# Optimization experiments

Hardware: AMD Instinct MI355X
Metric: run time of the kernel (lower is better)

The kernel has to match this reference:

```python
import jax, jax.numpy as jnp
import numpy as np

B, T, C = 4, 2048, 1024
N_HEAD = 16
HEAD = C // N_HEAD  # 64


def setup_inputs() -> dict:
    key = jax.random.key(0)
    k1, k2, k3 = jax.random.split(key, 3)
    x = jax.random.normal(k1, (B, T, C), dtype=jnp.float32)
    w_attn = jax.random.normal(k2, (C, 3 * C), dtype=jnp.float32) * (1.0 / np.sqrt(C))
    w_proj = jax.random.normal(k3, (C, C), dtype=jnp.float32) * (1.0 / np.sqrt(C))
    return {"x": x, "w_attn": w_attn, "w_proj": w_proj}


def reference(x, w_attn, w_proj):
    b, t, c = x.shape
    qkv = x @ w_attn  # [B,T,3C]
    q, k, v = jnp.split(qkv, 3, axis=-1)
    # [B,T,H,D] -> [B,H,T,D]
    q = q.reshape(b, t, N_HEAD, HEAD).transpose(0, 2, 1, 3)
    k = k.reshape(b, t, N_HEAD, HEAD).transpose(0, 2, 1, 3)
    v = v.reshape(b, t, N_HEAD, HEAD).transpose(0, 2, 1, 3)
    scale = 1.0 / np.sqrt(HEAD).astype(np.float32)
    attn = jnp.einsum('bhqd,bhkd->bhqk', q, k) * scale  # [B,H,T,T]
    causal = jnp.tril(jnp.ones((t, t), dtype=bool))
    attn = jnp.where(causal[None, None], attn, -jnp.inf)
    sm = jax.nn.softmax(attn, axis=-1)
    out = jnp.einsum('bhqk,bhkd->bhqd', sm, v)  # [B,H,T,D]
    out = out.transpose(0, 2, 1, 3).reshape(b, t, c)
    return out @ w_proj
```

## Files before the change

### kernel.cpp

```cpp
#include <hip/hip_runtime.h>
#include <stdint.h>

typedef unsigned short u16;
typedef __bf16 bf16x8 __attribute__((ext_vector_type(8)));
typedef float f32x4 __attribute__((ext_vector_type(4)));
typedef float f32x16 __attribute__((ext_vector_type(16)));

#define B_ 4
#define T_ 2048
#define C_ 1024
#define NH_ 16
#define HD_ 64
#define M_ (B_ * T_)
#define N1_ (3 * C_)
#define NQK_ 2048

__device__ inline u16 f2bf(float f) {
    uint32_t u = __float_as_uint(f);
    u += 0x7FFFu + ((u >> 16) & 1u);
    return (u16)(u >> 16);
}

__device__ inline bf16x8 ld_bf16x8(const u16* p) {
    return *(const bf16x8*)(const void*)p;
}

__device__ inline uint32_t cvtpk_bf16(float a, float b) {
    uint32_t r;
    asm("v_cvt_pk_bf16_f32 %0, %1, %2" : "=v"(r) : "v"(a), "v"(b));
    return r;
}

__device__ inline float exp2_fast(float x) {
    float r;
    asm("v_exp_f32 %0, %1" : "=v"(r) : "v"(x));
    return r;
}

__device__ inline void gload16(const u16* g, u16* l) {
    __builtin_amdgcn_global_load_lds(
        (const __attribute__((address_space(1))) uint32_t*)g,
        (__attribute__((address_space(3))) uint32_t*)l, 16, 0, 0);
}

__global__ void f32_to_bf16_k(const float* __restrict__ in, u16* __restrict__ out, int n) {
    int i = (blockIdx.x * blockDim.x + threadIdx.x) * 4;
    int stride = gridDim.x * blockDim.x * 4;
    for (; i < n; i += stride) {
        float4 v = *(const float4*)(in + i);
        uint2 o;
        o.x = (uint32_t)f2bf(v.x) | ((uint32_t)f2bf(v.y) << 16);
        o.y = (uint32_t)f2bf(v.z) | ((uint32_t)f2bf(v.w) << 16);
        *(uint2*)(out + i) = o;
    }
}

__global__ void transpose_f32_bf16_k(const float* __restrict__ in, u16* __restrict__ out,
                                     int R, int Cc, int scaleRows, float scale) {
    __shared__ float tile[32][33];
    int c0 = blockIdx.x * 32, r0 = blockIdx.y * 32;
    int tx = threadIdx.x, ty = threadIdx.y;
#pragma unroll
    for (int i = 0; i < 4; ++i)
        tile[ty + i * 8][tx] = in[(size_t)(r0 + ty + i * 8) * Cc + c0 + tx];
    __syncthreads();
#pragma unroll
    for (int i = 0; i < 4; ++i) {
        int orow = c0 + ty + i * 8;
        float v = tile[tx][ty + i * 8];
        if (orow < scaleRows) v *= scale;
        out[(size_t)orow * R + r0 + tx] = f2bf(v);
    }
}

template <int MODE>
__global__ __launch_bounds__(256) void gemm_bt_k(const u16* __restrict__ A,
                                                 const u16* __restrict__ Bt,
                                                 void* __restrict__ Cp,
                                                 u16* __restrict__ Vp,
                                                 int M, int N, int K) {
    __shared__ u16 As[128 * 32];
    __shared__ u16 Bs[128 * 32];
    const int t = threadIdx.x;
    const int w = t >> 6, l = t & 63;
    const int wr = w >> 1, wc = w & 1;
    const int lr = l & 15, lg = l >> 4;
    const int R0 = blockIdx.x * 128, C0 = blockIdx.y * 128;

    const int sr = t >> 2;
    const int sc = (t & 3) * 8;
    const u16* Ag  = A  + (size_t)(R0 + sr) * K + sc;
    const u16* Ag2 = Ag + (size_t)64 * K;
    const u16* Bg  = Bt + (size_t)(C0 + sr) * K + sc;
    const u16* Bg2 = Bg + (size_t)64 * K;

    f32x4 acc[4][4] = {};
    const int nk = K / 32;

    for (int kt = 0; kt < nk; ++kt) {
        __syncthreads();
        gload16(Ag  + (size_t)kt * 32, As + t * 8);
        gload16(Ag2 + (size_t)kt * 32, As + t * 8 + 2048);
        gload16(Bg  + (size_t)kt * 32, Bs + t * 8);
        gload16(Bg2 + (size_t)kt * 32, Bs + t * 8 + 2048);
        __syncthreads();

        bf16x8 af[4], bfr[4];
#pragma unroll
        for (int mi = 0; mi < 4; ++mi)
            af[mi] = ld_bf16x8(As + (wr * 64 + mi * 16 + lr) * 32 + lg * 8);
#pragma unroll
        for (int nj = 0; nj < 4; ++nj)
            bfr[nj] = ld_bf16x8(Bs + (wc * 64 + nj * 16 + lr) * 32 + lg * 8);
#pragma unroll
        for (int mi = 0; mi < 4; ++mi)
#pragma unroll
            for (int nj = 0; nj < 4; ++nj)
                acc[mi][nj] = __builtin_amdgcn_mfma_f32_16x16x32_bf16(af[mi], bfr[nj],
                                                                      acc[mi][nj], 0, 0, 0);
    }

    if (MODE == 2 && C0 >= 2048) {
#pragma unroll
        for (int mi = 0; mi < 4; ++mi) {
            int row = R0 + wr * 64 + mi * 16 + lg * 4;
            int bb = row >> 11, tt = row & 2047;
#pragma unroll
            for (int nj = 0; nj < 4; ++nj) {
                int cv = C0 - 2048 + wc * 64 + nj * 16 + lr;
                int hh = cv >> 6, dd = cv & 63;
                ushort4 pk;
                pk.x = f2bf(acc[mi][nj][0]);
                pk.y = f2bf(acc[mi][nj][1]);
                pk.z = f2bf(acc[mi][nj][2]);
                pk.w = f2bf(acc[mi][nj][3]);
                *(ushort4*)(Vp + (((size_t)bb * NH_ + hh) * HD_ + dd) * (size_t)T_ + tt) = pk;
            }
        }
    } else {
#pragma unroll
        for (int mi = 0; mi < 4; ++mi) {
            int row = R0 + wr * 64 + mi * 16 + lg * 4;
#pragma unroll
            for (int nj = 0; nj < 4; ++nj) {
                int col = C0 + wc * 64 + nj * 16 + lr;
#pragma unroll
                for (int r = 0; r < 4; ++r) {
                    if (MODE == 0)
                        ((float*)Cp)[(size_t)(row + r) * N + col] = acc[mi][nj][r];
                    else
                        ((u16*)Cp)[(size_t)(row + r) * NQK_ + col] = f2bf(acc[mi][nj][r]);
                }
            }
        }
    }
}

__global__ __launch_bounds__(256, 2) void attn_fwd_k(const u16* __restrict__ qk,
                                                     const u16* __restrict__ vT,
                                                     u16* __restrict__ attO) {
    __shared__ u16 Ks[2][64 * 64];
    __shared__ u16 Vs[2][64 * 64];

    const int t = threadIdx.x;
    const int w = t >> 6, l = t & 63;
    const int r0 = l & 31, hi = l >> 5;
    const int lin = blockIdx.x;
    const int bh = (lin & 7) * 8 + ((lin >> 3) & 7);
    const int pj = lin >> 6;
    const int b = bh >> 4, h = bh & 15;
    const u16* qkB = qk + (size_t)b * T_ * NQK_;

    const int sr = t >> 3;
    const int sof = ((t & 7) * 8) ^ ((sr & 7) << 3);
    const u16* gK = qkB + (size_t)sr * NQK_ + C_ + h * HD_ + sof;
    const u16* gV = vT + ((size_t)bh * HD_ + sr) * (size_t)T_ + sof;

    for (int jj = 0; jj < 2; ++jj) {
        const int J = jj ? pj : (15 - pj);
        const int qW = J * 128 + w * 32;
        const int nt = 2 * J + 2;

        bf16x8 qf[4];
        {
            const u16* qp = qkB + (size_t)(qW + r0) * NQK_ + h * HD_ + hi * 8;
#pragma unroll
            for (int dc = 0; dc < 4; ++dc) qf[dc] = ld_bf16x8(qp + dc * 16);
        }

        f32x16 acc0 = {}, acc1 = {};
        float m = -1e30f, lsum = 0.f;

        gload16(gK, Ks[0] + t * 8);
        gload16(gK + (size_t)32 * NQK_, Ks[0] + t * 8 + 2048);
        gload16(gV, Vs[0] + t * 8);
        gload16(gV + (size_t)32 * T_, Vs[0] + t * 8 + 2048);
        __syncthreads();

        for (int kt = 0; kt < nt; ++kt) {
            const int kv = kt * 64;
            if (kt + 1 < nt) {
                u16* dK = Ks[(kt + 1) & 1];
                u16* dV = Vs[(kt + 1) & 1];
                gload16(gK + (size_t)(kv + 64) * NQK_, dK + t * 8);
                gload16(gK + (size_t)(kv + 96) * NQK_, dK + t * 8 + 2048);
                gload16(gV + (kv + 64), dV + t * 8);
                gload16(gV + (size_t)32 * T_ + (kv + 64), dV + t * 8 + 2048);
            }
            const u16* Kb = Ks[kt & 1];
            const u16* Vb = Vs[kt & 1];

            if (kv <= qW) {
                const bool diag = (kv + 64 > qW);
                const bool up = (!diag) || (w & 1);

                f32x16 s0 = {}, s1 = {};
                __builtin_amdgcn_s_setprio(1);
#pragma unroll
                for (int dc = 0; dc < 4; ++dc) {
                    int off = (dc * 32 + hi * 16) ^ ((r0 & 7) << 4);
                    bf16x8 k0 = ld_bf16x8((const u16*)((const char*)Kb + r0 * 128 + off));
                    s0 = __builtin_amdgcn_mfma_f32_32x32x16_bf16(k0, qf[dc], s0, 0, 0, 0);
                    if (up) {
                        bf16x8 k1 = ld_bf16x8((const u16*)((const char*)Kb + r0 * 128 + 4096 + off));
                        s1 = __builtin_amdgcn_mfma_f32_32x32x16_bf16(k1, qf[dc], s1, 0, 0, 0);
                    }
                }
                __builtin_amdgcn_s_setprio(0);

                if (diag) {
                    int qrel = qW + r0 - kv;
#pragma unroll
                    for (int rg = 0; rg < 16; ++rg) {
                        int kv0 = (rg & 3) + 8 * (rg >> 2) + hi * 4;
                        s0[rg] = (kv0 > qrel) ? -1e30f : s0[rg];
                        if (up) s1[rg] = (kv0 + 32 > qrel) ? -1e30f : s1[rg];
                    }
                }

                float a4[8];
                if (up) {
#pragma unroll
                    for (int i = 0; i < 8; ++i)
                        a4[i] = fmaxf(fmaxf(s0[i], s0[i + 8]), fmaxf(s1[i], s1[i + 8]));
                } else {
#pragma unroll
                    for (int i = 0; i < 8; ++i) a4[i] = fmaxf(s0[i], s0[i + 8]);
                }
#pragma unroll
                for (int i = 0; i < 4; ++i) a4[i] = fmaxf(a4[i], a4[i + 4]);
                float mx = fmaxf(fmaxf(a4[0], a4[1]), fmaxf(a4[2], a4[3]));
                mx = fmaxf(mx, __shfl_xor(mx, 32));

                if (!__all(mx - m <= 8.f)) {
                    float mn = fmaxf(m, mx);
                    float corr = exp2_fast(m - mn);
                    m = mn;
                    lsum *= corr;
#pragma unroll
                    for (int rg = 0; rg < 16; ++rg) { acc0[rg] *= corr; acc1[rg] *= corr; }
                }
#pragma unroll
                for (int rg = 0; rg < 16; ++rg) s0[rg] = exp2_fast(s0[rg] - m);
                if (up) {
#pragma unroll
                    for (int rg = 0; rg < 16; ++rg) s1[rg] = exp2_fast(s1[rg] - m);
                }
                float sb[8];
                if (up) {
#pragma unroll
                    for (int i = 0; i < 8; ++i) sb[i] = (s0[i] + s0[i + 8]) + (s1[i] + s1[i + 8]);
                } else {
#pragma unroll
                    for (int i = 0; i < 8; ++i) sb[i] = s0[i] + s0[i + 8];
                }
#pragma unroll
                for (int i = 0; i < 4; ++i) sb[i] += sb[i + 4];
                float rs = (sb[0] + sb[1]) + (sb[2] + sb[3]);
                rs += __shfl_xor(rs, 32);
                lsum += rs;

                bf16x8 pb0, pb1, pb2, pb3;
                {
                    uint32_t c0 = cvtpk_bf16(s0[0], s0[1]),   c1 = cvtpk_bf16(s0[2], s0[3]);
                    uint32_t c2 = cvtpk_bf16(s0[4], s0[5]),   c3 = cvtpk_bf16(s0[6], s0[7]);
                    uint32_t c4 = cvtpk_bf16(s0[8], s0[9]),   c5 = cvtpk_bf16(s0[10], s0[11]);
                    uint32_t c6 = cvtpk_bf16(s0[12], s0[13]), c7 = cvtpk_bf16(s0[14], s0[15]);
                    uint32_t x0 = (uint32_t)__shfl_xor((int)c0, 32), x1 = (uint32_t)__shfl_xor((int)c1, 32);
                    uint32_t x2 = (uint32_t)__shfl_xor((int)c2, 32), x3 = (uint32_t)__shfl_xor((int)c3, 32);
                    uint32_t x4 = (uint32_t)__shfl_xor((int)c4, 32), x5 = (uint32_t)__shfl_xor((int)c5, 32);
                    uint32_t x6 = (uint32_t)__shfl_xor((int)c6, 32), x7 = (uint32_t)__shfl_xor((int)c7, 32);
                    union { uint32_t u[4]; bf16x8 v; } f0, f1;
                    f0.u[0] = hi ? x2 : c0;  f0.u[1] = hi ? x3 : c1;
                    f0.u[2] = hi ? c2 : x0;  f0.u[3] = hi ? c3 : x1;
                    f1.u[0] = hi ? x6 : c4;  f1.u[1] = hi ? x7 : c5;
                    f1.u[2] = hi ? c6 : x4;  f1.u[3] = hi ? c7 : x5;
                    pb0 = f0.v; pb1 = f1.v;
                }
                if (up) {
                    uint32_t c0 = cvtpk_bf16(s1[0], s1[1]),   c1 = cvtpk_bf16(s1[2], s1[3]);
                    uint32_t c2 = cvtpk_bf16(s1[4], s1[5]),   c3 = cvtpk_bf16(s1[6], s1[7]);
                    uint32_t c4 = cvtpk_bf16(s1[8], s1[9]),   c5 = cvtpk_bf16(s1[10], s1[11]);
                    uint32_t c6 = cvtpk_bf16(s1[12], s1[13]), c7 = cvtpk_bf16(s1[14], s1[15]);
                    uint32_t x0 = (uint32_t)__shfl_xor((int)c0, 32), x1 = (uint32_t)__shfl_xor((int)c1, 32);
                    uint32_t x2 = (uint32_t)__shfl_xor((int)c2, 32), x3 = (uint32_t)__shfl_xor((int)c3, 32);
                    uint32_t x4 = (uint32_t)__shfl_xor((int)c4, 32), x5 = (uint32_t)__shfl_xor((int)c5, 32);
                    uint32_t x6 = (uint32_t)__shfl_xor((int)c6, 32), x7 = (uint32_t)__shfl_xor((int)c7, 32);
                    union { uint32_t u[4]; bf16x8 v; } f0, f1;
                    f0.u[0] = hi ? x2 : c0;  f0.u[1] = hi ? x3 : c1;
                    f0.u[2] = hi ? c2 : x0;  f0.u[3] = hi ? c3 : x1;
                    f1.u[0] = hi ? x6 : c4;  f1.u[1] = hi ? x7 : c5;
                    f1.u[2] = hi ? c6 : x4;  f1.u[3] = hi ? c7 : x5;
                    pb2 = f0.v; pb3 = f1.v;
                }

                __builtin_amdgcn_s_setprio(1);
                {
                    int off0 = (hi * 16) ^ ((r0 & 7) << 4);
                    int off1 = (32 + hi * 16) ^ ((r0 & 7) << 4);
                    bf16x8 va0 = ld_bf16x8((const u16*)((const char*)Vb + r0 * 128 + off0));
                    bf16x8 va1 = ld_bf16x8((const u16*)((const char*)Vb + r0 * 128 + off1));
                    bf16x8 vb0 = ld_bf16x8((const u16*)((const char*)Vb + r0 * 128 + 4096 + off0));
                    bf16x8 vb1 = ld_bf16x8((const u16*)((const char*)Vb + r0 * 128 + 4096 + off1));
                    acc0 = __builtin_amdgcn_mfma_f32_32x32x16_bf16(va0, pb0, acc0, 0, 0, 0);
                    acc0 = __builtin_amdgcn_mfma_f32_32x32x16_bf16(va1, pb1, acc0, 0, 0, 0);
                    acc1 = __builtin_amdgcn_mfma_f32_32x32x16_bf16(vb0, pb0, acc1, 0, 0, 0);
                    acc1 = __builtin_amdgcn_mfma_f32_32x32x16_bf16(vb1, pb1, acc1, 0, 0, 0);
                    if (up) {
                        int off2 = (64 + hi * 16) ^ ((r0 & 7) << 4);
                        int off3 = (96 + hi * 16) ^ ((r0 & 7) << 4);
                        bf16x8 va2 = ld_bf16x8((const u16*)((const char*)Vb + r0 * 128 + off2));
                        bf16x8 va3 = ld_bf16x8((const u16*)((const char*)Vb + r0 * 128 + off3));
                        bf16x8 vb2 = ld_bf16x8((const u16*)((const char*)Vb + r0 * 128 + 4096 + off2));
                        bf16x8 vb3 = ld_bf16x8((const u16*)((const char*)Vb + r0 * 128 + 4096 + off3));
                        acc0 = __builtin_amdgcn_mfma_f32_32x32x16_bf16(va2, pb2, acc0, 0, 0, 0);
                        acc0 = __builtin_amdgcn_mfma_f32_32x32x16_bf16(va3, pb3, acc0, 0, 0, 0);
                        acc1 = __builtin_amdgcn_mfma_f32_32x32x16_bf16(vb2, pb2, acc1, 0, 0, 0);
                        acc1 = __builtin_amdgcn_mfma_f32_32x32x16_bf16(vb3, pb3, acc1, 0, 0, 0);
                    }
                }
                __builtin_amdgcn_s_setprio(0);
            }

            __syncthreads();
        }

        float inv = 1.0f / lsum;
        u16* op = attO + ((size_t)b * T_ + qW + r0) * C_ + h * HD_;
#pragma unroll
        for (int g = 0; g < 4; ++g) {
            int d0 = g * 8 + hi * 4;
            ushort4 p0, p1;
            p0.x = f2bf(acc0[4 * g + 0] * inv);
            p0.y = f2bf(acc0[4 * g + 1] * inv);
            p0.z = f2bf(acc0[4 * g + 2] * inv);
            p0.w = f2bf(acc0[4 * g + 3] * inv);
            *(ushort4*)(op + d0) = p0;
            p1.x = f2bf(acc1[4 * g + 0] * inv);
            p1.y = f2bf(acc1[4 * g + 1] * inv);
            p1.z = f2bf(acc1[4 * g + 2] * inv);
            p1.w = f2bf(acc1[4 * g + 3] * inv);
            *(ushort4*)(op + 32 + d0) = p1;
        }
    }
}

extern "C" void kernel_launch(void* const* d_in, const int* in_sizes, int n_in,
                              void* d_out, int out_size, void* d_ws, size_t ws_size,
                              hipStream_t stream) {
    const float* x      = (const float*)d_in[0];
    const float* w_attn = (const float*)d_in[1];
    const float* w_proj = (const float*)d_in[2];
    float* out = (float*)d_out;

    char* ws = (char*)d_ws;
    const size_t SZ_XB = (size_t)M_ * C_ * 2;
    const size_t SZ_WA = (size_t)C_ * N1_ * 2;
    const size_t SZ_WP = (size_t)C_ * C_ * 2;
    const size_t SZ_QK = (size_t)M_ * NQK_ * 2;
    const size_t SZ_VT = (size_t)M_ * C_ * 2;
    u16* xb   = (u16*)ws;
    u16* waT  = (u16*)(ws + SZ_XB);
    u16* wpT  = (u16*)(ws + SZ_XB + SZ_WA);
    u16* qkb  = (u16*)(ws + SZ_XB + SZ_WA + SZ_WP);
    u16* vtb  = (u16*)(ws + SZ_XB + SZ_WA + SZ_WP + SZ_QK);
    u16* attO = (u16*)(ws + SZ_XB + SZ_WA + SZ_WP + SZ_QK + SZ_VT);

    f32_to_bf16_k<<<2048, 256, 0, stream>>>(x, xb, M_ * C_);
    dim3 tb(32, 8);
    transpose_f32_bf16_k<<<dim3(N1_ / 32, C_ / 32), tb, 0, stream>>>(w_attn, waT, C_, N1_, C_,
                                                                     0.125f * 1.44269504088896f);
    transpose_f32_bf16_k<<<dim3(C_ / 32, C_ / 32), tb, 0, stream>>>(w_proj, wpT, C_, C_, 0, 1.0f);

    gemm_bt_k<2><<<dim3(M_ / 128, N1_ / 128), 256, 0, stream>>>(xb, waT, qkb, vtb, M_, N1_, C_);
    attn_fwd_k<<<dim3(512), 256, 0, stream>>>(qkb, vtb, attO);
    gemm_bt_k<0><<<dim3(M_ / 128, C_ / 128), 256, 0, stream>>>(attO, wpT, out, nullptr, M_, C_, C_);
}
```

Baseline: 201.3 us.

## Triple-buffer GEMM LDS tiles with async global-to-LDS prefetch two stages ahead

The bf16 GEMM main loop moves from a single LDS buffer with two barriers per k-step to a three-stage ring buffer. Tiles are prefetched two iterations ahead, with a manual vmcnt wait and one barrier per iteration. The MFMA block is also wrapped in s_setprio to favour matrix issue. This is meant to hide global-load latency behind compute, at the cost of three times the LDS per block, which could reduce occupancy.

```diff
diff --git a/kernel.cpp b/kernel.cpp
--- a/kernel.cpp
+++ b/kernel.cpp
@@ -79,8 +79,8 @@
                                                  void* __restrict__ Cp,
                                                  u16* __restrict__ Vp,
                                                  int M, int N, int K) {
-    __shared__ u16 As[128 * 32];
-    __shared__ u16 Bs[128 * 32];
+    __shared__ u16 As[3][128 * 32];
+    __shared__ u16 Bs[3][128 * 32];
     const int t = threadIdx.x;
     const int w = t >> 6, l = t & 63;
     const int wr = w >> 1, wc = w & 1;
@@ -97,28 +97,48 @@
     f32x4 acc[4][4] = {};
     const int nk = K / 32;
 
+#define STAGE(KT, BI)                                               \
+    do {                                                            \
+        gload16(Ag  + (size_t)(KT) * 32, As[BI] + t * 8);           \
+        gload16(Ag2 + (size_t)(KT) * 32, As[BI] + t * 8 + 2048);    \
+        gload16(Bg  + (size_t)(KT) * 32, Bs[BI] + t * 8);           \
+        gload16(Bg2 + (size_t)(KT) * 32, Bs[BI] + t * 8 + 2048);    \
+    } while (0)
+
+    STAGE(0, 0);
+    if (nk > 1) STAGE(1, 1);
+
+    int bi = 0;
     for (int kt = 0; kt < nk; ++kt) {
-        __syncthreads();
-        gload16(Ag  + (size_t)kt * 32, As + t * 8);
-        gload16(Ag2 + (size_t)kt * 32, As + t * 8 + 2048);
-        gload16(Bg  + (size_t)kt * 32, Bs + t * 8);
-        gload16(Bg2 + (size_t)kt * 32, Bs + t * 8 + 2048);
-        __syncthreads();
-
+        if (kt + 1 < nk) asm volatile("s_waitcnt vmcnt(4)" ::: "memory");
+        else             asm volatile("s_waitcnt vmcnt(0)" ::: "memory");
+        __builtin_amdgcn_s_barrier();
+        __builtin_amdgcn_sched_barrier(0);
+        if (kt + 2 < nk) {
+            int bn = bi + 2; if (bn >= 3) bn -= 3;
+            STAGE(kt + 2, bn);
+        }
+
+        const u16* Ab = As[bi];
+        const u16* Bb = Bs[bi];
         bf16x8 af[4], bfr[4];
 #pragma unroll
         for (int mi = 0; mi < 4; ++mi)
-            af[mi] = ld_bf16x8(As + (wr * 64 + mi * 16 + lr) * 32 + lg * 8);
+            af[mi] = ld_bf16x8(Ab + (wr * 64 + mi * 16 + lr) * 32 + lg * 8);
 #pragma unroll
         for (int nj = 0; nj < 4; ++nj)
-            bfr[nj] = ld_bf16x8(Bs + (wc * 64 + nj * 16 + lr) * 32 + lg * 8);
+            bfr[nj] = ld_bf16x8(Bb + (wc * 64 + nj * 16 + lr) * 32 + lg * 8);
+        __builtin_amdgcn_s_setprio(1);
 #pragma unroll
         for (int mi = 0; mi < 4; ++mi)
 #pragma unroll
             for (int nj = 0; nj < 4; ++nj)
                 acc[mi][nj] = __builtin_amdgcn_mfma_f32_16x16x32_bf16(af[mi], bfr[nj],
                                                                       acc[mi][nj], 0, 0, 0);
+        __builtin_amdgcn_s_setprio(0);
+        bi = (bi + 1 == 3) ? 0 : bi + 1;
     }
+#undef STAGE
 
     if (MODE == 2 && C0 >= 2048) {
 #pragma unroll
```

Result: faster. 192.5 us (-4.4%).
